# Kernel optimization log

Hardware: AMD Instinct MI355X
Metric: run time of the kernel (lower is better)

## Reference

```python
import math
import jax, jax.numpy as jnp
import numpy as np

NUM_HEADS = 12
ALPHA, BETA, GAMMA = 1.9, 3.8, 15.2  # get_rpe_config(ratio=1.9)
SKIP = 1


def _rp_bucket(side):
    """iRPE euclidean contextual bucket table for a side x side grid + 1 cls token."""
    beta_int = int(BETA)
    coords = np.stack(np.meshgrid(np.arange(side), np.arange(side), indexing='ij'), -1).reshape(-1, 2)
    diff = coords[:, None, :] - coords[None, :, :]
    dis = np.round(np.sqrt((diff ** 2).sum(-1).astype(np.float64)))  # rounded euclidean distance
    far = np.clip(np.round(ALPHA + np.log(np.maximum(dis, 1e-9) / ALPHA) / math.log(GAMMA / ALPHA) * (BETA - ALPHA)), None, BETA)
    idx = np.where(dis <= ALPHA, dis, far).astype(np.int32) + beta_int
    num_buckets = 2 * beta_int + 1  # 7
    L = side * side
    full = np.full((L + SKIP, L + SKIP), num_buckets, dtype=np.int32)  # extra bucket for cls
    full[SKIP:, SKIP:] = idx
    return full, num_buckets + 1  # table [P,P], total buckets = 8


def setup_inputs() -> dict:
    key = jax.random.key(0)
    ks = jax.random.split(key, 8)
    B, P, n_mod, C = 64, 197, 2, 768
    N = 1 + (P - 1) * n_mod  # 393
    hd = C // NUM_HEADS
    rp_bucket, n_buckets = _rp_bucket(int(math.sqrt(P - SKIP)))
    s = 0.02
    return {
        'x': jax.random.normal(ks[0], (B, N, C), jnp.float32),
        'q_learned': jax.random.normal(ks[1], (1, 1, C), jnp.float32) * s,
        'pos_embed': jax.random.normal(ks[2], (1, P, C), jnp.float32) * s,
        'wk': jax.random.normal(ks[3], (C, C), jnp.float32) * s,
        'wv': jax.random.normal(ks[4], (C, C), jnp.float32) * s,
        'rpe_w': jax.random.normal(ks[5], (hd, n_buckets), jnp.float32) * s,  # shared_head ctx lookup table
        'proj_w': jax.random.normal(ks[6], (C, C), jnp.float32) * s,
        'proj_b': jnp.zeros((C,), jnp.float32),
        'rp_bucket': jnp.asarray(rp_bucket),  # [P, P] int32
    }


def reference(x, q_learned, pos_embed, wk, wv, rpe_w, proj_w, proj_b, rp_bucket):
    B, N, C = x.shape
    H = NUM_HEADS
    hd = C // H
    P = rp_bucket.shape[0]
    n_mod = (N - 1) // (P - 1)
    scale = hd ** -0.5

    q_ = jnp.broadcast_to(q_learned + pos_embed, (B, P, C))
    q = q_.reshape(B, P, H, hd).transpose(0, 2, 1, 3)                    # bhpd
    k = (x @ wk.T).reshape(B, N, H, hd).transpose(0, 2, 1, 3)            # bhnd
    v = (x @ wv.T).reshape(B, N, H, hd).transpose(0, 2, 1, 3)            # bhnd

    attn = jnp.einsum('bhpd,bhnd->bhpn', q, k) * scale                   # [B,H,P,N]

    # contextual RPE on keys: lookup = q @ table, gathered by rp_bucket[i, j]
    lookup = jnp.einsum('bhpd,du->bhpu', q, rpe_w)                        # [B,H,P,n_buckets]
    bias = lookup[:, :, jnp.arange(P)[:, None], rp_bucket]                # [B,H,P,P]
    bias = jnp.concatenate([bias[..., :1], jnp.tile(bias[..., 1:], (1, 1, 1, n_mod))], axis=-1)
    attn = jax.nn.softmax(attn + bias, axis=-1)

    out = jnp.einsum('bhpn,bhnd->bhpd', attn, v).transpose(0, 2, 1, 3).reshape(B, P, C)
    return out @ proj_w.T + proj_b
```

## Files before the change

kernel.cpp:

```cpp
#include <hip/hip_runtime.h>

typedef unsigned short u16;
typedef short bf16x8 __attribute__((ext_vector_type(8)));
typedef float f32x4 __attribute__((ext_vector_type(4)));
typedef const __attribute__((address_space(1))) void* gptr_t;
typedef __attribute__((address_space(3))) void* lptr_t;

#define B_   64
#define N_   393
#define C_   768
#define H_   12
#define HD_  64
#define P_   197
#define BIAS_N 416
#define PPAD 208
#define VTP  448
#define M_KV (B_ * N_)
#define M_PR (B_ * P_)
#define SCALE_L2E 0.180336879f

__device__ __forceinline__ u16 f2bf(float f) {
    unsigned u = __float_as_uint(f);
    return (u16)((u + 0x7FFFu + ((u >> 16) & 1u)) >> 16);
}
__device__ __forceinline__ unsigned cvt_pk_bf16(float lo, float hi) {
    unsigned r;
    asm("v_cvt_pk_bf16_f32 %0, %1, %2" : "=v"(r) : "v"(lo), "v"(hi));
    return r;
}
__device__ __forceinline__ float exp2_fast(float x) {
    float r;
    asm("v_exp_f32 %0, %1" : "=v"(r) : "v"(x));
    return r;
}

__global__ __launch_bounds__(256) void conv_prep1(
    const float* __restrict__ x, const float* __restrict__ wk,
    const float* __restrict__ wv, const float* __restrict__ pw,
    const float* __restrict__ q_learned, const float* __restrict__ pos_embed,
    const float* __restrict__ rpe_w,
    u16* __restrict__ xh, u16* __restrict__ wkvh, u16* __restrict__ pwh,
    u16* __restrict__ qh, float* __restrict__ lk)
{
    __shared__ float q_s[C_];
    const int bx = blockIdx.x, t = threadIdx.x;
    if (bx < 20592) {
        const int XN4 = 19316736 / 4;
        const int WN4 = 589824 / 4;
        int i = bx * 256 + t;
        const float* src; u16* dst; int off;
        if (i < XN4) { src = x; dst = xh; off = i; }
        else {
            int j = i - XN4;
            int sec = j / WN4;
            off = j - sec * WN4;
            src = sec == 0 ? wk : (sec == 1 ? wv : pw);
            dst = sec == 0 ? wkvh : (sec == 1 ? wkvh + 589824 : pwh);
        }
        float4 v = ((const float4*)src)[off];
        u16 o[4] = {f2bf(v.x), f2bf(v.y), f2bf(v.z), f2bf(v.w)};
        *(uint2*)(dst + off * 4) = *(uint2*)o;
    } else {
        const int p = bx - 20592;
        for (int c = t; c < C_; c += 256) {
            float v = q_learned[c] + pos_embed[p * C_ + c];
            q_s[c] = v;
            qh[p * C_ + c] = f2bf(v);
        }
        __syncthreads();
        if (t < H_ * 8) {
            int h = t >> 3, u = t & 7;
            float s = 0.f;
            #pragma unroll 8
            for (int d = 0; d < HD_; ++d)
                s = fmaf(q_s[h * HD_ + d], rpe_w[d * 8 + u], s);
            lk[(h * P_ + p) * 8 + u] = s;
        }
    }
}

template <bool F32OUT>
__global__ __launch_bounds__(256) void gemm_bf16(
    const u16* __restrict__ A, const u16* __restrict__ Bw,
    u16* __restrict__ Cb, float* __restrict__ Cf, const float* __restrict__ bias,
    int M, int ldc)
{
    __shared__ __align__(16) u16 As[128 * 64];
    __shared__ __align__(16) u16 Bs[128 * 64];

    const int gx = gridDim.x;
    const int nwg = gx * gridDim.y;
    const int orig = blockIdx.y * gx + blockIdx.x;
    const int xcd = orig & 7, rank = orig >> 3;
    const int q = nwg >> 3, r = nwg & 7;
    const int wgid = (xcd < r ? xcd * (q + 1) : r * (q + 1) + (xcd - r) * q) + rank;
    const int n0 = (wgid % gx) * 128;
    const int m0 = (wgid / gx) * 128;

    const int t = threadIdx.x;
    const int w = t >> 6, l = t & 63;
    const int wr = w >> 1, wc = w & 1;
    const int l15 = l & 15, lg = l >> 4;
    const int lrow = l >> 3, lslot = l & 7;
    const int Mc = M - 1;

    f32x4 acc[4][4];
    #pragma unroll
    for (int i = 0; i < 4; ++i)
        #pragma unroll
        for (int j = 0; j < 4; ++j) acc[i][j] = (f32x4){0.f, 0.f, 0.f, 0.f};

    for (int ks = 0; ks < 12; ++ks) {
        const int k0 = ks * 64;
        if (ks) __syncthreads();
        #pragma unroll
        for (int i = 0; i < 4; ++i) {
            const int rbase = w * 32 + i * 8;
            int arow = m0 + rbase + lrow; if (arow > Mc) arow = Mc;
            const int brow = n0 + rbase + lrow;
            const u16* ga = A  + (size_t)arow * 768 + k0 + lslot * 8;
            const u16* gb = Bw + (size_t)brow * 768 + k0 + lslot * 8;
            __builtin_amdgcn_global_load_lds((gptr_t)(const void*)ga,
                                             (lptr_t)(void*)(As + rbase * 64), 16, 0, 0);
            __builtin_amdgcn_global_load_lds((gptr_t)(const void*)gb,
                                             (lptr_t)(void*)(Bs + rbase * 64), 16, 0, 0);
        }
        __syncthreads();
        #pragma unroll
        for (int kk = 0; kk < 2; ++kk) {
            bf16x8 af[4], bfr[4];
            #pragma unroll
            for (int mf = 0; mf < 4; ++mf) {
                af[mf]  = *(const bf16x8*)(As + (wr * 64 + mf * 16 + l15) * 64 + (kk * 4 + lg) * 8);
                bfr[mf] = *(const bf16x8*)(Bs + (wc * 64 + mf * 16 + l15) * 64 + (kk * 4 + lg) * 8);
            }
            #pragma unroll
            for (int mf = 0; mf < 4; ++mf)
                #pragma unroll
                for (int nf = 0; nf < 4; ++nf)
                    acc[mf][nf] = __builtin_amdgcn_mfma_f32_16x16x32_bf16(
                        af[mf], bfr[nf], acc[mf][nf], 0, 0, 0);
        }
    }

    #pragma unroll
    for (int mf = 0; mf < 4; ++mf) {
        #pragma unroll
        for (int nf = 0; nf < 4; ++nf) {
            int col = n0 + wc * 64 + nf * 16 + l15;
            float bb = 0.f;
            if (F32OUT) bb = bias[col];
            #pragma unroll
            for (int rr = 0; rr < 4; ++rr) {
                int m = m0 + wr * 64 + mf * 16 + lg * 4 + rr;
                if (m < M) {
                    if (F32OUT) Cf[(size_t)m * ldc + col] = acc[mf][nf][rr] + bb;
                    else        Cb[(size_t)m * ldc + col] = f2bf(acc[mf][nf][rr]);
                }
            }
        }
    }
}

__global__ __launch_bounds__(256) void vtrans_prep2(
    const u16* __restrict__ KV, u16* __restrict__ Vt,
    const float* __restrict__ lk, const int* __restrict__ rp_bucket,
    float* __restrict__ biasT)
{
    __shared__ __align__(16) u16 vts[64][68];
    const int bx = blockIdx.x, t = threadIdx.x;
    if (bx < B_ * H_) {
        const int b = bx / H_, h = bx % H_;
        const u16* src = KV + (size_t)b * N_ * 1536 + 768 + h * HD_;
        u16* dst = Vt + (size_t)bx * HD_ * VTP;
        for (int jt = 0; jt < 7; ++jt) {
            const int j0 = jt * 64;
            if (jt) __syncthreads();
            #pragma unroll
            for (int ps = 0; ps < 2; ++ps) {
                int jr = ps * 32 + (t >> 3);
                int dd = (t & 7) * 8;
                int j = j0 + jr;
                bf16x8 v = (bf16x8){0, 0, 0, 0, 0, 0, 0, 0};
                if (j < N_) v = *(const bf16x8*)(src + (size_t)j * 1536 + dd);
                *(bf16x8*)(&vts[jr][dd]) = v;
            }
            __syncthreads();
            #pragma unroll
            for (int ps = 0; ps < 2; ++ps) {
                int idx = t + 256 * ps;
                int d = idx >> 3, ch = idx & 7;
                u16 v[8];
                #pragma unroll
                for (int k = 0; k < 8; ++k) v[k] = vts[ch * 8 + k][d];
                *(bf16x8*)(dst + (size_t)d * VTP + j0 + ch * 8) = *(bf16x8*)v;
            }
        }
    } else {
        const int i = bx - B_ * H_;
        const int h = i / N_, j = i % N_;
        if (t >= PPAD) return;
        int jm;
        if (j == 0) jm = 0;
        else { jm = j - 1; if (jm >= 196) jm -= 196; jm += 1; }
        float v = 0.f;
        if (t < P_) {
            int bucket = rp_bucket[t * P_ + jm];
            v = lk[(h * P_ + t) * 8 + bucket] * 1.44269504f;
        }
        biasT[((size_t)h * BIAS_N + j) * PPAD + t] = v;
    }
}

__global__ __launch_bounds__(256, 2) void attn_mfma5(
    const u16* __restrict__ qh, const u16* __restrict__ KV,
    const u16* __restrict__ Vt, const float* __restrict__ biasT,
    u16* __restrict__ Obuf)
{
    __shared__ __align__(16) u16 pts[64 * 456];
    __shared__ __align__(16) u16 kvs[2][64 * 64];

    const int id = blockIdx.x;
    const int work = (id & 7) * 384 + (id >> 3);
    const int ptile = work & 3;
    const int rest = work >> 2;
    const int h = rest % 12;
    const int b = rest / 12;
    const int p0 = ptile * 64;

    const int t = threadIdx.x, w = t >> 6, l = t & 63;
    const int l15 = l & 15, lg = l >> 4;
    const int p0w = p0 + w * 16;

    int srow[2], sslot[2], swoff[2];
    #pragma unroll
    for (int i = 0; i < 2; ++i) {
        int c = t + 256 * i;
        srow[i] = c >> 3; sslot[i] = c & 7;
        swoff[i] = srow[i] * 64 + ((sslot[i] ^ (srow[i] & 7)) << 3);
    }

    int prow = p0w + l15; if (prow > P_ - 1) prow = P_ - 1;
    const u16* qp = qh + (size_t)prow * C_ + h * HD_ + lg * 8;
    bf16x8 qf0 = *(const bf16x8*)(qp);
    bf16x8 qf1 = *(const bf16x8*)(qp + 32);

    const u16* Kbase = KV + (size_t)b * (N_ * 1536) + h * HD_;
    const u16* Vbase = Vt + (size_t)(b * H_ + h) * (HD_ * VTP);

    f32x4 acc[7][4];
    #pragma unroll
    for (int i = 0; i < 7; ++i)
        #pragma unroll
        for (int j = 0; j < 4; ++j) acc[i][j] = (f32x4){0.f, 0.f, 0.f, 0.f};

    bf16x8 ra[2];
    #pragma unroll
    for (int i = 0; i < 2; ++i)
        ra[i] = *(const bf16x8*)(Kbase + (size_t)srow[i] * 1536 + sslot[i] * 8);
    #pragma unroll
    for (int i = 0; i < 2; ++i) *(bf16x8*)(&kvs[0][swoff[i]]) = ra[i];
    __syncthreads();

    #pragma unroll
    for (int nt = 0; nt < 7; ++nt) {
        const u16* kcur = kvs[nt & 1];
        if (nt < 6) {
            #pragma unroll
            for (int i = 0; i < 2; ++i) {
                int rn = (nt + 1) * 64 + srow[i]; if (rn > N_ - 1) rn = N_ - 1;
                ra[i] = *(const bf16x8*)(Kbase + (size_t)rn * 1536 + sslot[i] * 8);
            }
        }
        const int smax = (nt == 6) ? 1 : 4;
        __builtin_amdgcn_s_setprio(1);
        #pragma unroll
        for (int kc = 0; kc < 2; ++kc)
            #pragma unroll
            for (int sub = 0; sub < smax; ++sub) {
                int row = sub * 16 + l15;
                bf16x8 kb = *(const bf16x8*)(kcur + row * 64 + (((kc * 4 + lg) ^ (row & 7)) << 3));
                acc[nt][sub] = __builtin_amdgcn_mfma_f32_16x16x32_bf16(
                    kc ? qf1 : qf0, kb, acc[nt][sub], 0, 0, 0);
            }
        __builtin_amdgcn_s_setprio(0);
        if (nt < 6) {
            #pragma unroll
            for (int i = 0; i < 2; ++i) *(bf16x8*)(&kvs[(nt + 1) & 1][swoff[i]]) = ra[i];
        }
        __syncthreads();
    }

    #pragma unroll
    for (int i = 0; i < 2; ++i)
        ra[i] = *(const bf16x8*)(Vbase + (size_t)srow[i] * VTP + sslot[i] * 8);

    const int pcl = (p0w + lg * 4) > (PPAD - 4) ? (PPAD - 4) : (p0w + lg * 4);
    float s4[4] = {0.f, 0.f, 0.f, 0.f};
    #pragma unroll
    for (int nt = 0; nt < 7; ++nt) {
        const int smax = (nt == 6) ? 1 : 4;
        #pragma unroll
        for (int sub = 0; sub < smax; ++sub) {
            int n = nt * 64 + sub * 16 + l15;
            if (n < N_) {
                float4 b4 = *(const float4*)(biasT + ((size_t)h * BIAS_N + n) * PPAD + pcl);
                float bb[4] = {b4.x, b4.y, b4.z, b4.w};
                #pragma unroll
                for (int rr = 0; rr < 4; ++rr) {
                    float e = exp2_fast(fmaf(acc[nt][sub][rr], SCALE_L2E, bb[rr]));
                    acc[nt][sub][rr] = e;
                    s4[rr] += e;
                }
            } else {
                acc[nt][sub] = (f32x4){0.f, 0.f, 0.f, 0.f};
            }
        }
    }
    float rinv4[4];
    #pragma unroll
    for (int rr = 0; rr < 4; ++rr) {
        float s = s4[rr];
        s += __shfl_xor(s, 1); s += __shfl_xor(s, 2);
        s += __shfl_xor(s, 4); s += __shfl_xor(s, 8);
        rinv4[rr] = 1.0f / s;
    }

    {
        const int rowb = w * 16 + lg * 4;
        #pragma unroll
        for (int nt = 0; nt < 7; ++nt) {
            const int smax = (nt == 6) ? 1 : 4;
            #pragma unroll
            for (int sub = 0; sub < smax; ++sub) {
                int col = nt * 64 + sub * 16 + l15;
                unsigned pk01 = cvt_pk_bf16(acc[nt][sub][0], acc[nt][sub][1]);
                unsigned pk23 = cvt_pk_bf16(acc[nt][sub][2], acc[nt][sub][3]);
                pts[(rowb + 0) * 456 + col] = (u16)pk01;
                pts[(rowb + 1) * 456 + col] = (u16)(pk01 >> 16);
                pts[(rowb + 2) * 456 + col] = (u16)pk23;
                pts[(rowb + 3) * 456 + col] = (u16)(pk23 >> 16);
            }
        }
        #pragma unroll
        for (int rr = 0; rr < 4; ++rr)
            pts[(rowb + rr) * 456 + 400 + l15] = 0;
    }
    #pragma unroll
    for (int i = 0; i < 2; ++i) *(bf16x8*)(&kvs[0][swoff[i]]) = ra[i];
    __syncthreads();

    f32x4 o[4];
    #pragma unroll
    for (int i = 0; i < 4; ++i) o[i] = (f32x4){0.f, 0.f, 0.f, 0.f};

    #pragma unroll
    for (int nt = 0; nt < 7; ++nt) {
        const u16* kcur = kvs[nt & 1];
        if (nt < 6) {
            #pragma unroll
            for (int i = 0; i < 2; ++i)
                ra[i] = *(const bf16x8*)(Vbase + (size_t)srow[i] * VTP + (nt + 1) * 64 + sslot[i] * 8);
        }
        const int kcmax = (nt == 6) ? 1 : 2;
        __builtin_amdgcn_s_setprio(1);
        #pragma unroll
        for (int kc = 0; kc < kcmax; ++kc) {
            bf16x8 pa = *(const bf16x8*)(pts + (w * 16 + l15) * 456 + nt * 64 + kc * 32 + lg * 8);
            #pragma unroll
            for (int dsub = 0; dsub < 4; ++dsub) {
                int row = dsub * 16 + l15;
                bf16x8 vb = *(const bf16x8*)(kcur + row * 64 + (((kc * 4 + lg) ^ (row & 7)) << 3));
                o[dsub] = __builtin_amdgcn_mfma_f32_16x16x32_bf16(pa, vb, o[dsub], 0, 0, 0);
            }
        }
        __builtin_amdgcn_s_setprio(0);
        if (nt < 6) {
            #pragma unroll
            for (int i = 0; i < 2; ++i) *(bf16x8*)(&kvs[(nt + 1) & 1][swoff[i]]) = ra[i];
        }
        __syncthreads();
    }

    #pragma unroll
    for (int dsub = 0; dsub < 4; ++dsub)
        #pragma unroll
        for (int rr = 0; rr < 4; ++rr) {
            int p = p0w + lg * 4 + rr;
            if (p < P_)
                Obuf[((size_t)b * P_ + p) * C_ + h * HD_ + dsub * 16 + l15] =
                    f2bf(o[dsub][rr] * rinv4[rr]);
        }
}

extern "C" void kernel_launch(void* const* d_in, const int* in_sizes, int n_in,
                              void* d_out, int out_size, void* d_ws, size_t ws_size,
                              hipStream_t stream)
{
    const float* x         = (const float*)d_in[0];
    const float* q_learned = (const float*)d_in[1];
    const float* pos_embed = (const float*)d_in[2];
    const float* wk        = (const float*)d_in[3];
    const float* wv        = (const float*)d_in[4];
    const float* rpe_w     = (const float*)d_in[5];
    const float* proj_w    = (const float*)d_in[6];
    const float* proj_b    = (const float*)d_in[7];
    const int*   rp_bucket = (const int*)d_in[8];
    float* out = (float*)d_out;

    char* ws = (char*)d_ws;
    u16*   xh    = (u16*)(ws);
    u16*   wkvh  = (u16*)(ws + 38633472);
    u16*   pwh   = (u16*)(ws + 40992768);
    u16*   qh    = (u16*)(ws + 42172416);
    float* lk    = (float*)(ws + 42475008);
    float* biasT = (float*)(ws + 42550784);
    u16*   KV    = (u16*)(ws + 46704128);
    u16*   Vt    = (u16*)(ws + 123971072);
    u16*   Obuf  = (u16*)(ws + 168011264);

    conv_prep1<<<20789, 256, 0, stream>>>(x, wk, wv, proj_w,
                                          q_learned, pos_embed, rpe_w,
                                          xh, wkvh, pwh, qh, lk);

    dim3 gkv(1536 / 128, (M_KV + 127) / 128);
    gemm_bf16<false><<<gkv, 256, 0, stream>>>(xh, wkvh, KV, nullptr, nullptr, M_KV, 1536);

    vtrans_prep2<<<5484, 256, 0, stream>>>(KV, Vt, lk, rp_bucket, biasT);

    attn_mfma5<<<3072, 256, 0, stream>>>(qh, KV, Vt, biasT, Obuf);

    dim3 gpr(768 / 128, (M_PR + 127) / 128);
    gemm_bf16<true><<<gpr, 256, 0, stream>>>(Obuf, pwh, nullptr, out, proj_b, M_PR, 768);
}
```

Measured before the change: 228.0 us.

## Fuse QK, softmax and PV per key tile in a flash-style attention loop

The attention kernel no longer keeps all seven QK score tiles in registers and a full 64x456 probability tile in LDS. It now computes one 64-key tile of scores, exponentiates it, writes it to a small LDS tile and immediately multiplies by V. MFMA operands are swapped so each lane owns one query row, and the bias table is transposed to query-major so each row reads its bias contiguously. The goal is lower register and LDS use so four blocks fit per CU instead of two, with K and V loads overlapped inside one loop. The cost is an extra barrier per tile and a single-row sum reduction across lanes. The unnormalized exp without max subtraction is kept as before.

```diff
diff --git a/kernel.cpp b/kernel.cpp
--- a/kernel.cpp
+++ b/kernel.cpp
@@ -18,6 +18,7 @@
 #define M_KV (B_ * N_)
 #define M_PR (B_ * P_)
 #define SCALE_L2E 0.180336879f
+#define PPITCH 70
 
 __device__ __forceinline__ u16 f2bf(float f) {
     unsigned u = __float_as_uint(f);
@@ -165,7 +166,7 @@
 __global__ __launch_bounds__(256) void vtrans_prep2(
     const u16* __restrict__ KV, u16* __restrict__ Vt,
     const float* __restrict__ lk, const int* __restrict__ rp_bucket,
-    float* __restrict__ biasT)
+    float* __restrict__ biasT2)
 {
     __shared__ __align__(16) u16 vts[64][68];
     const int bx = blockIdx.x, t = threadIdx.x;
@@ -198,27 +199,29 @@
         }
     } else {
         const int i = bx - B_ * H_;
-        const int h = i / N_, j = i % N_;
-        if (t >= PPAD) return;
-        int jm;
-        if (j == 0) jm = 0;
-        else { jm = j - 1; if (jm >= 196) jm -= 196; jm += 1; }
-        float v = 0.f;
-        if (t < P_) {
-            int bucket = rp_bucket[t * P_ + jm];
-            v = lk[(h * P_ + t) * 8 + bucket] * 1.44269504f;
-        }
-        biasT[((size_t)h * BIAS_N + j) * PPAD + t] = v;
-    }
-}
-
-__global__ __launch_bounds__(256, 2) void attn_mfma5(
+        const int h = i / PPAD, p = i % PPAD;
+        for (int j = t; j < BIAS_N; j += 256) {
+            float v = 0.f;
+            if (p < P_ && j < N_) {
+                int jm;
+                if (j == 0) jm = 0;
+                else { jm = j - 1; if (jm >= 196) jm -= 196; jm += 1; }
+                int bucket = rp_bucket[p * P_ + jm];
+                v = lk[(h * P_ + p) * 8 + bucket] * 1.44269504f;
+            }
+            biasT2[((size_t)h * PPAD + p) * BIAS_N + j] = v;
+        }
+    }
+}
+
+__global__ __launch_bounds__(256, 4) void attn_flash(
     const u16* __restrict__ qh, const u16* __restrict__ KV,
-    const u16* __restrict__ Vt, const float* __restrict__ biasT,
+    const u16* __restrict__ Vt, const float* __restrict__ biasT2,
     u16* __restrict__ Obuf)
 {
-    __shared__ __align__(16) u16 pts[64 * 456];
-    __shared__ __align__(16) u16 kvs[2][64 * 64];
+    __shared__ __align__(16) u16 kk[2][64 * 64];
+    __shared__ __align__(16) u16 vv[64 * 64];
+    __shared__ __align__(16) u16 pp[64 * PPITCH];
 
     const int id = blockIdx.x;
     const int work = (id & 7) * 384 + (id >> 3);
@@ -231,6 +234,7 @@
     const int t = threadIdx.x, w = t >> 6, l = t & 63;
     const int l15 = l & 15, lg = l >> 4;
     const int p0w = p0 + w * 16;
+    const int rowp = w * 16 + l15;
 
     int srow[2], sslot[2], swoff[2];
     #pragma unroll
@@ -247,150 +251,112 @@
 
     const u16* Kbase = KV + (size_t)b * (N_ * 1536) + h * HD_;
     const u16* Vbase = Vt + (size_t)(b * H_ + h) * (HD_ * VTP);
-
-    f32x4 acc[7][4];
-    #pragma unroll
-    for (int i = 0; i < 7; ++i)
-        #pragma unroll
-        for (int j = 0; j < 4; ++j) acc[i][j] = (f32x4){0.f, 0.f, 0.f, 0.f};
-
-    bf16x8 ra[2];
+    const int pcl = (p0 + rowp) > (PPAD - 1) ? (PPAD - 1) : (p0 + rowp);
+    const float* bias_row = biasT2 + ((size_t)h * PPAD + pcl) * BIAS_N;
+
+    bf16x8 raK[2], raV[2];
     #pragma unroll
     for (int i = 0; i < 2; ++i)
-        ra[i] = *(const bf16x8*)(Kbase + (size_t)srow[i] * 1536 + sslot[i] * 8);
-    #pragma unroll
-    for (int i = 0; i < 2; ++i) *(bf16x8*)(&kvs[0][swoff[i]]) = ra[i];
+        raK[i] = *(const bf16x8*)(Kbase + (size_t)srow[i] * 1536 + sslot[i] * 8);
+    #pragma unroll
+    for (int i = 0; i < 2; ++i) *(bf16x8*)(&kk[0][swoff[i]]) = raK[i];
+    #pragma unroll
+    for (int i = 0; i < 2; ++i)
+        raV[i] = *(const bf16x8*)(Vbase + (size_t)srow[i] * VTP + sslot[i] * 8);
     __syncthreads();
 
+    float s_acc = 0.f;
+    f32x4 o[4];
+    #pragma unroll
+    for (int i = 0; i < 4; ++i) o[i] = (f32x4){0.f, 0.f, 0.f, 0.f};
+
     #pragma unroll
     for (int nt = 0; nt < 7; ++nt) {
-        const u16* kcur = kvs[nt & 1];
+        const u16* kcur = kk[nt & 1];
+
+        f32x4 accs[4];
+        #pragma unroll
+        for (int i = 0; i < 4; ++i) accs[i] = (f32x4){0.f, 0.f, 0.f, 0.f};
+        __builtin_amdgcn_s_setprio(1);
+        #pragma unroll
+        for (int kc = 0; kc < 2; ++kc)
+            #pragma unroll
+            for (int sub = 0; sub < 4; ++sub) {
+                int row = sub * 16 + l15;
+                bf16x8 kb = *(const bf16x8*)(kcur + row * 64 + (((kc * 4 + lg) ^ (row & 7)) << 3));
+                accs[sub] = __builtin_amdgcn_mfma_f32_16x16x32_bf16(
+                    kb, kc ? qf1 : qf0, accs[sub], 0, 0, 0);
+            }
+        __builtin_amdgcn_s_setprio(0);
+
+        #pragma unroll
+        for (int i = 0; i < 2; ++i) *(bf16x8*)(&vv[swoff[i]]) = raV[i];
         if (nt < 6) {
             #pragma unroll
             for (int i = 0; i < 2; ++i) {
                 int rn = (nt + 1) * 64 + srow[i]; if (rn > N_ - 1) rn = N_ - 1;
-                ra[i] = *(const bf16x8*)(Kbase + (size_t)rn * 1536 + sslot[i] * 8);
-            }
-        }
-        const int smax = (nt == 6) ? 1 : 4;
-        __builtin_amdgcn_s_setprio(1);
-        #pragma unroll
-        for (int kc = 0; kc < 2; ++kc)
-            #pragma unroll
-            for (int sub = 0; sub < smax; ++sub) {
-                int row = sub * 16 + l15;
-                bf16x8 kb = *(const bf16x8*)(kcur + row * 64 + (((kc * 4 + lg) ^ (row & 7)) << 3));
-                acc[nt][sub] = __builtin_amdgcn_mfma_f32_16x16x32_bf16(
-                    kc ? qf1 : qf0, kb, acc[nt][sub], 0, 0, 0);
-            }
-        __builtin_amdgcn_s_setprio(0);
-        if (nt < 6) {
-            #pragma unroll
-            for (int i = 0; i < 2; ++i) *(bf16x8*)(&kvs[(nt + 1) & 1][swoff[i]]) = ra[i];
+                raK[i] = *(const bf16x8*)(Kbase + (size_t)rn * 1536 + sslot[i] * 8);
+            }
+        }
+
+        #pragma unroll
+        for (int sub = 0; sub < 4; ++sub) {
+            int jb = nt * 64 + sub * 16 + lg * 4;
+            float4 b4 = *(const float4*)(bias_row + jb);
+            float bb[4] = {b4.x, b4.y, b4.z, b4.w};
+            float e[4];
+            #pragma unroll
+            for (int rr = 0; rr < 4; ++rr) {
+                float ev = exp2_fast(fmaf(accs[sub][rr], SCALE_L2E, bb[rr]));
+                e[rr] = (jb + rr < N_) ? ev : 0.f;
+                s_acc += e[rr];
+            }
+            unsigned pk01 = cvt_pk_bf16(e[0], e[1]);
+            unsigned pk23 = cvt_pk_bf16(e[2], e[3]);
+            *(unsigned*)(&pp[rowp * PPITCH + sub * 16 + lg * 4]) = pk01;
+            *(unsigned*)(&pp[rowp * PPITCH + sub * 16 + lg * 4 + 2]) = pk23;
         }
         __syncthreads();
-    }
-
-    #pragma unroll
-    for (int i = 0; i < 2; ++i)
-        ra[i] = *(const bf16x8*)(Vbase + (size_t)srow[i] * VTP + sslot[i] * 8);
-
-    const int pcl = (p0w + lg * 4) > (PPAD - 4) ? (PPAD - 4) : (p0w + lg * 4);
-    float s4[4] = {0.f, 0.f, 0.f, 0.f};
-    #pragma unroll
-    for (int nt = 0; nt < 7; ++nt) {
-        const int smax = (nt == 6) ? 1 : 4;
-        #pragma unroll
-        for (int sub = 0; sub < smax; ++sub) {
-            int n = nt * 64 + sub * 16 + l15;
-            if (n < N_) {
-                float4 b4 = *(const float4*)(biasT + ((size_t)h * BIAS_N + n) * PPAD + pcl);
-                float bb[4] = {b4.x, b4.y, b4.z, b4.w};
-                #pragma unroll
-                for (int rr = 0; rr < 4; ++rr) {
-                    float e = exp2_fast(fmaf(acc[nt][sub][rr], SCALE_L2E, bb[rr]));
-                    acc[nt][sub][rr] = e;
-                    s4[rr] += e;
-                }
-            } else {
-                acc[nt][sub] = (f32x4){0.f, 0.f, 0.f, 0.f};
-            }
-        }
-    }
-    float rinv4[4];
-    #pragma unroll
-    for (int rr = 0; rr < 4; ++rr) {
-        float s = s4[rr];
-        s += __shfl_xor(s, 1); s += __shfl_xor(s, 2);
-        s += __shfl_xor(s, 4); s += __shfl_xor(s, 8);
-        rinv4[rr] = 1.0f / s;
-    }
-
-    {
-        const int rowb = w * 16 + lg * 4;
-        #pragma unroll
-        for (int nt = 0; nt < 7; ++nt) {
-            const int smax = (nt == 6) ? 1 : 4;
-            #pragma unroll
-            for (int sub = 0; sub < smax; ++sub) {
-                int col = nt * 64 + sub * 16 + l15;
-                unsigned pk01 = cvt_pk_bf16(acc[nt][sub][0], acc[nt][sub][1]);
-                unsigned pk23 = cvt_pk_bf16(acc[nt][sub][2], acc[nt][sub][3]);
-                pts[(rowb + 0) * 456 + col] = (u16)pk01;
-                pts[(rowb + 1) * 456 + col] = (u16)(pk01 >> 16);
-                pts[(rowb + 2) * 456 + col] = (u16)pk23;
-                pts[(rowb + 3) * 456 + col] = (u16)(pk23 >> 16);
-            }
-        }
-        #pragma unroll
-        for (int rr = 0; rr < 4; ++rr)
-            pts[(rowb + rr) * 456 + 400 + l15] = 0;
-    }
-    #pragma unroll
-    for (int i = 0; i < 2; ++i) *(bf16x8*)(&kvs[0][swoff[i]]) = ra[i];
-    __syncthreads();
-
-    f32x4 o[4];
-    #pragma unroll
-    for (int i = 0; i < 4; ++i) o[i] = (f32x4){0.f, 0.f, 0.f, 0.f};
-
-    #pragma unroll
-    for (int nt = 0; nt < 7; ++nt) {
-        const u16* kcur = kvs[nt & 1];
-        if (nt < 6) {
-            #pragma unroll
-            for (int i = 0; i < 2; ++i)
-                ra[i] = *(const bf16x8*)(Vbase + (size_t)srow[i] * VTP + (nt + 1) * 64 + sslot[i] * 8);
-        }
+
         const int kcmax = (nt == 6) ? 1 : 2;
         __builtin_amdgcn_s_setprio(1);
         #pragma unroll
         for (int kc = 0; kc < kcmax; ++kc) {
-            bf16x8 pa = *(const bf16x8*)(pts + (w * 16 + l15) * 456 + nt * 64 + kc * 32 + lg * 8);
+            bf16x8 pa = *(const bf16x8*)(&pp[rowp * PPITCH + kc * 32 + lg * 8]);
             #pragma unroll
             for (int dsub = 0; dsub < 4; ++dsub) {
                 int row = dsub * 16 + l15;
-                bf16x8 vb = *(const bf16x8*)(kcur + row * 64 + (((kc * 4 + lg) ^ (row & 7)) << 3));
-                o[dsub] = __builtin_amdgcn_mfma_f32_16x16x32_bf16(pa, vb, o[dsub], 0, 0, 0);
+                bf16x8 vb = *(const bf16x8*)(vv + row * 64 + (((kc * 4 + lg) ^ (row & 7)) << 3));
+                o[dsub] = __builtin_amdgcn_mfma_f32_16x16x32_bf16(vb, pa, o[dsub], 0, 0, 0);
             }
         }
         __builtin_amdgcn_s_setprio(0);
+
         if (nt < 6) {
             #pragma unroll
-            for (int i = 0; i < 2; ++i) *(bf16x8*)(&kvs[(nt + 1) & 1][swoff[i]]) = ra[i];
+            for (int i = 0; i < 2; ++i) *(bf16x8*)(&kk[(nt + 1) & 1][swoff[i]]) = raK[i];
+            #pragma unroll
+            for (int i = 0; i < 2; ++i)
+                raV[i] = *(const bf16x8*)(Vbase + (size_t)srow[i] * VTP + (nt + 1) * 64 + sslot[i] * 8);
         }
         __syncthreads();
     }
 
-    #pragma unroll
-    for (int dsub = 0; dsub < 4; ++dsub)
-        #pragma unroll
-        for (int rr = 0; rr < 4; ++rr) {
-            int p = p0w + lg * 4 + rr;
-            if (p < P_)
-                Obuf[((size_t)b * P_ + p) * C_ + h * HD_ + dsub * 16 + l15] =
-                    f2bf(o[dsub][rr] * rinv4[rr]);
-        }
+    s_acc += __shfl_xor(s_acc, 16);
+    s_acc += __shfl_xor(s_acc, 32);
+    float rinv = 1.0f / s_acc;
+
+    int p = p0 + rowp;
+    if (p < P_) {
+        #pragma unroll
+        for (int dsub = 0; dsub < 4; ++dsub) {
+            u16 v4[4];
+            #pragma unroll
+            for (int rr = 0; rr < 4; ++rr) v4[rr] = f2bf(o[dsub][rr] * rinv);
+            *(uint2*)(Obuf + ((size_t)b * P_ + p) * C_ + h * HD_ + dsub * 16 + lg * 4) =
+                *(uint2*)v4;
+        }
+    }
 }
 
 extern "C" void kernel_launch(void* const* d_in, const int* in_sizes, int n_in,
@@ -414,7 +380,7 @@
     u16*   pwh   = (u16*)(ws + 40992768);
     u16*   qh    = (u16*)(ws + 42172416);
     float* lk    = (float*)(ws + 42475008);
-    float* biasT = (float*)(ws + 42550784);
+    float* biasT2= (float*)(ws + 42550784);
     u16*   KV    = (u16*)(ws + 46704128);
     u16*   Vt    = (u16*)(ws + 123971072);
     u16*   Obuf  = (u16*)(ws + 168011264);
@@ -426,9 +392,9 @@
     dim3 gkv(1536 / 128, (M_KV + 127) / 128);
     gemm_bf16<false><<<gkv, 256, 0, stream>>>(xh, wkvh, KV, nullptr, nullptr, M_KV, 1536);
 
-    vtrans_prep2<<<5484, 256, 0, stream>>>(KV, Vt, lk, rp_bucket, biasT);
-
-    attn_mfma5<<<3072, 256, 0, stream>>>(qh, KV, Vt, biasT, Obuf);
+    vtrans_prep2<<<3264, 256, 0, stream>>>(KV, Vt, lk, rp_bucket, biasT2);
+
+    attn_flash<<<3072, 256, 0, stream>>>(qh, KV, Vt, biasT2, Obuf);
 
     dim3 gpr(768 / 128, (M_PR + 127) / 128);
     gemm_bf16<true><<<gpr, 256, 0, stream>>>(Obuf, pwh, nullptr, out, proj_b, M_PR, 768);
```

New measurement: 214.7 us. 1.06x faster.
